# Performance work log

Hardware: AMD Instinct MI355X
Metric: run time of the kernel (lower is better)

## Reference

```python
import jax, jax.numpy as jnp
import numpy as np

B, TQ, TV, D = 8, 256, 512, 128
LN_EPS = 1e-3  # Keras LayerNormalization default epsilon


def setup_inputs() -> dict:
    key = jax.random.key(0)
    k1, k2, k3 = jax.random.split(key, 3)
    x = jax.random.normal(k1, (B, TQ, D), dtype=jnp.float32)
    context = jax.random.normal(k2, (B, TV, D), dtype=jnp.float32)
    scale = jax.random.normal(k3, (D,), dtype=jnp.float32)  # AdditiveAttention use_scale vector
    gamma = jnp.ones((D,), dtype=jnp.float32)
    beta = jnp.zeros((D,), dtype=jnp.float32)
    return {"x": x, "context": context, "scale": scale, "gamma": gamma, "beta": beta}


def reference(x, context, scale, gamma, beta):
    # Bahdanau additive attention: scores[b,i,j] = sum_d scale[d]*tanh(x[b,i,d] + context[b,j,d])
    # [B,TQ,TV,D] broadcasted intermediate, contracted over d with the learned scale vector.
    scores = jnp.einsum("bijd,d->bij", jnp.tanh(x[:, :, None, :] + context[:, None, :, :]), scale)
    weights = jax.nn.softmax(scores, axis=-1)          # [B,TQ,TV]
    attn_out = jnp.einsum("bij,bjd->bid", weights, context)  # weighted sum of values (=context)
    # residual add + LayerNorm over last axis
    y = x + attn_out
    mu = jnp.mean(y, axis=-1, keepdims=True)
    var = jnp.mean(jnp.square(y - mu), axis=-1, keepdims=True)
    out = gamma * (y - mu) * jax.lax.rsqrt(var + LN_EPS) + beta
    return out
```

## Files before the change

### kernel.cpp

```cpp
#include <hip/hip_runtime.h>
#include <math.h>

#define BB 8
#define TQ 256
#define TV 512
#define DD 128
#define TI 4
#define NT 1024
#define LN_EPS 1e-3f

typedef float f4 __attribute__((ext_vector_type(4)));

__global__ __launch_bounds__(256) void prep_kernel(const float* __restrict__ ctx,
                                                   float* __restrict__ F) {
    int idx = blockIdx.x * 256 + threadIdx.x;
    f4 c = ((const f4*)ctx)[idx];
    f4 r;
#pragma unroll
    for (int k = 0; k < 4; ++k) r[k] = __expf(2.0f * c[k]);
    ((f4*)F)[idx] = r;
}

__global__ __launch_bounds__(NT, 8) void attn_kernel(const float* __restrict__ x,
                                                     const float* __restrict__ ctx,
                                                     const float* __restrict__ scale,
                                                     const float* __restrict__ gamma,
                                                     const float* __restrict__ beta,
                                                     const float* __restrict__ F,
                                                     float* __restrict__ out) {
    __shared__ float xs[TI * DD];
    __shared__ f4    txE[DD];
    __shared__ float s2n[DD];
    __shared__ f4    pacc[TV];
    __shared__ f4    wT[TV];
    __shared__ float red[8][TI][DD];
    __shared__ f4    mred[8];
    __shared__ f4    sred[8];
    __shared__ float lnred[8][2];

    const int t  = threadIdx.x;
    const int bg = blockIdx.x;
    const int wg   = (bg & 7) * 64 + (bg >> 3);
    const int b    = wg >> 6;
    const int i0   = (wg & 63) * TI;
    const int wv   = t >> 6;
    const int lane = t & 63;

    if (t < TI * DD) {
        int r = t >> 7, d = t & 127;
        float v = x[(size_t)(b * TQ + i0 + r) * DD + d];
        xs[t] = v;
        txE[d][r] = __expf(2.0f * v);
    }
    if (t >= 512 && t < 512 + DD) s2n[t - 512] = -2.0f * scale[t - 512];
    __syncthreads();

    const int j = t & 511;
    const int h = t >> 9;
    f4 acc = {0.f, 0.f, 0.f, 0.f};
    {
        const f4* Fp = (const f4*)(F + (size_t)(b * TV + j) * DD + h * 64);
#pragma unroll 2
        for (int d4 = 0; d4 < 16; ++d4) {
            f4 Fv = Fp[d4];
#pragma unroll
            for (int k = 0; k < 4; ++k) {
                const int d = h * 64 + d4 * 4 + k;
                f4 E = txE[d];
                float sn = s2n[d];
                f4 den, u;
#pragma unroll
                for (int r = 0; r < TI; ++r) den[r] = fmaf(E[r], Fv[k], 1.0f);
#pragma unroll
                for (int r = 0; r < TI; ++r) u[r] = __builtin_amdgcn_rcpf(den[r]);
#pragma unroll
                for (int r = 0; r < TI; ++r) acc[r] = fmaf(sn, u[r], acc[r]);
            }
        }
    }
    if (h == 1) pacc[j] = acc;
    __syncthreads();
    if (h == 0) {
        f4 o = pacc[j];
#pragma unroll
        for (int r = 0; r < TI; ++r) acc[r] += o[r];
    }

    f4 m = acc;
#pragma unroll
    for (int off = 32; off > 0; off >>= 1) {
#pragma unroll
        for (int r = 0; r < TI; ++r) m[r] = fmaxf(m[r], __shfl_xor(m[r], off));
    }
    if (lane == 0 && wv < 8) mred[wv] = m;
    __syncthreads();
    f4 M = mred[0];
#pragma unroll
    for (int w = 1; w < 8; ++w) {
        f4 o = mred[w];
#pragma unroll
        for (int r = 0; r < TI; ++r) M[r] = fmaxf(M[r], o[r]);
    }
    f4 e;
#pragma unroll
    for (int r = 0; r < TI; ++r) e[r] = __expf(acc[r] - M[r]);
    f4 s = e;
#pragma unroll
    for (int off = 32; off > 0; off >>= 1) {
#pragma unroll
        for (int r = 0; r < TI; ++r) s[r] += __shfl_xor(s[r], off);
    }
    if (lane == 0 && wv < 8) sred[wv] = s;
    __syncthreads();
    f4 S = sred[0];
#pragma unroll
    for (int w = 1; w < 8; ++w) {
        f4 o = sred[w];
#pragma unroll
        for (int r = 0; r < TI; ++r) S[r] += o[r];
    }
    if (h == 0) {
        f4 w4;
#pragma unroll
        for (int r = 0; r < TI; ++r) w4[r] = e[r] * __builtin_amdgcn_rcpf(S[r]);
        wT[j] = w4;
    }
    __syncthreads();

    {
        const int g = t >> 7;
        const int d = t & 127;
        const float* cp = ctx + (size_t)(b * TV + g * 64) * DD + d;
        f4 p = {0.f, 0.f, 0.f, 0.f};
#pragma unroll 4
        for (int jj = 0; jj < 64; ++jj) {
            f4 wj = wT[g * 64 + jj];
            float cv = cp[(size_t)jj * DD];
#pragma unroll
            for (int r = 0; r < TI; ++r) p[r] = fmaf(wj[r], cv, p[r]);
        }
#pragma unroll
        for (int r = 0; r < TI; ++r) red[g][r][d] = p[r];
    }
    __syncthreads();

    {
        const int r = t >> 7;
        const int d = t & 127;
        float y = 0.f;
        if (t < 512) {
            float attn = 0.f;
#pragma unroll
            for (int g = 0; g < 8; ++g) attn += red[g][r][d];
            y = xs[r * DD + d] + attn;
        }
        float s1 = y, s2 = y * y;
#pragma unroll
        for (int off = 32; off > 0; off >>= 1) {
            s1 += __shfl_xor(s1, off);
            s2 += __shfl_xor(s2, off);
        }
        if (lane == 0 && wv < 8) { lnred[wv][0] = s1; lnred[wv][1] = s2; }
        __syncthreads();
        if (t < 512) {
            float S1 = lnred[2 * r][0] + lnred[2 * r + 1][0];
            float S2 = lnred[2 * r][1] + lnred[2 * r + 1][1];
            float mu  = S1 * (1.0f / 128.0f);
            float var = S2 * (1.0f / 128.0f) - mu * mu;
            float inv = rsqrtf(var + LN_EPS);
            out[(size_t)(b * TQ + i0 + r) * DD + d] = gamma[d] * (y - mu) * inv + beta[d];
        }
    }
}

extern "C" void kernel_launch(void* const* d_in, const int* in_sizes, int n_in,
                              void* d_out, int out_size, void* d_ws, size_t ws_size,
                              hipStream_t stream) {
    const float* x     = (const float*)d_in[0];
    const float* ctx   = (const float*)d_in[1];
    const float* scale = (const float*)d_in[2];
    const float* gamma = (const float*)d_in[3];
    const float* beta  = (const float*)d_in[4];
    float* out = (float*)d_out;

    float* F = (float*)d_ws;

    prep_kernel<<<(BB * TV * DD / 4) / 256, 256, 0, stream>>>(ctx, F);
    attn_kernel<<<(BB * TQ) / TI, NT, 0, stream>>>(x, ctx, scale, gamma, beta, F, out);
}
```

Before: 90.91 us.

## Combine four reciprocals into one via common denominator and restructure score split

Groups four d-terms per step and sums their reciprocal contributions over a shared denominator, so one rcp replaces four at the cost of extra multiplies and FMAs. The score work is also re-split: each thread handles two j positions over a quarter of D instead of one j over half of D, with a four-way partial reduction through shared memory. Softmax is reduced only in the first four waves using an online max/sum rescale, which removes one block barrier. The product of four denominators (each 1+e^{2x}e^{2c}) can overflow float range for large inputs, which risks inf/NaN or lost precision.

```diff
diff --git a/kernel.cpp b/kernel.cpp
--- a/kernel.cpp
+++ b/kernel.cpp
@@ -10,6 +10,28 @@
 #define LN_EPS 1e-3f
 
 typedef float f4 __attribute__((ext_vector_type(4)));
+
+static __device__ __forceinline__ f4 vfma_s(f4 a, float s, f4 c) {
+    f4 r;
+    r[0] = fmaf(a[0], s, c[0]); r[1] = fmaf(a[1], s, c[1]);
+    r[2] = fmaf(a[2], s, c[2]); r[3] = fmaf(a[3], s, c[3]);
+    return r;
+}
+static __device__ __forceinline__ f4 vfma_v(f4 a, f4 b, f4 c) {
+    f4 r;
+    r[0] = fmaf(a[0], b[0], c[0]); r[1] = fmaf(a[1], b[1], c[1]);
+    r[2] = fmaf(a[2], b[2], c[2]); r[3] = fmaf(a[3], b[3], c[3]);
+    return r;
+}
+static __device__ __forceinline__ f4 vmul_s(f4 a, float s) {
+    f4 r; r[0] = a[0]*s; r[1] = a[1]*s; r[2] = a[2]*s; r[3] = a[3]*s; return r;
+}
+static __device__ __forceinline__ f4 vrcp(f4 a) {
+    f4 r;
+    r[0] = __builtin_amdgcn_rcpf(a[0]); r[1] = __builtin_amdgcn_rcpf(a[1]);
+    r[2] = __builtin_amdgcn_rcpf(a[2]); r[3] = __builtin_amdgcn_rcpf(a[3]);
+    return r;
+}
 
 __global__ __launch_bounds__(256) void prep_kernel(const float* __restrict__ ctx,
                                                    float* __restrict__ F) {
@@ -30,12 +52,12 @@
                                                      float* __restrict__ out) {
     __shared__ float xs[TI * DD];
     __shared__ f4    txE[DD];
-    __shared__ float s2n[DD];
-    __shared__ f4    pacc[TV];
+    __shared__ f4    s2n4[DD / 4];
+    __shared__ f4    pacc[3][256][2];
     __shared__ f4    wT[TV];
     __shared__ float red[8][TI][DD];
-    __shared__ f4    mred[8];
-    __shared__ f4    sred[8];
+    __shared__ f4    mred[4];
+    __shared__ f4    sred[4];
     __shared__ float lnred[8][2];
 
     const int t  = threadIdx.x;
@@ -52,78 +74,103 @@
         xs[t] = v;
         txE[d][r] = __expf(2.0f * v);
     }
-    if (t >= 512 && t < 512 + DD) s2n[t - 512] = -2.0f * scale[t - 512];
-    __syncthreads();
-
-    const int j = t & 511;
-    const int h = t >> 9;
-    f4 acc = {0.f, 0.f, 0.f, 0.f};
-    {
-        const f4* Fp = (const f4*)(F + (size_t)(b * TV + j) * DD + h * 64);
-#pragma unroll 2
-        for (int d4 = 0; d4 < 16; ++d4) {
-            f4 Fv = Fp[d4];
-#pragma unroll
-            for (int k = 0; k < 4; ++k) {
-                const int d = h * 64 + d4 * 4 + k;
-                f4 E = txE[d];
-                float sn = s2n[d];
-                f4 den, u;
-#pragma unroll
-                for (int r = 0; r < TI; ++r) den[r] = fmaf(E[r], Fv[k], 1.0f);
-#pragma unroll
-                for (int r = 0; r < TI; ++r) u[r] = __builtin_amdgcn_rcpf(den[r]);
-#pragma unroll
-                for (int r = 0; r < TI; ++r) acc[r] = fmaf(sn, u[r], acc[r]);
-            }
-        }
-    }
-    if (h == 1) pacc[j] = acc;
-    __syncthreads();
-    if (h == 0) {
-        f4 o = pacc[j];
-#pragma unroll
-        for (int r = 0; r < TI; ++r) acc[r] += o[r];
-    }
-
-    f4 m = acc;
-#pragma unroll
-    for (int off = 32; off > 0; off >>= 1) {
-#pragma unroll
-        for (int r = 0; r < TI; ++r) m[r] = fmaxf(m[r], __shfl_xor(m[r], off));
-    }
-    if (lane == 0 && wv < 8) mred[wv] = m;
-    __syncthreads();
-    f4 M = mred[0];
-#pragma unroll
-    for (int w = 1; w < 8; ++w) {
-        f4 o = mred[w];
-#pragma unroll
-        for (int r = 0; r < TI; ++r) M[r] = fmaxf(M[r], o[r]);
-    }
-    f4 e;
-#pragma unroll
-    for (int r = 0; r < TI; ++r) e[r] = __expf(acc[r] - M[r]);
-    f4 s = e;
-#pragma unroll
-    for (int off = 32; off > 0; off >>= 1) {
-#pragma unroll
-        for (int r = 0; r < TI; ++r) s[r] += __shfl_xor(s[r], off);
-    }
-    if (lane == 0 && wv < 8) sred[wv] = s;
-    __syncthreads();
-    f4 S = sred[0];
-#pragma unroll
-    for (int w = 1; w < 8; ++w) {
-        f4 o = sred[w];
-#pragma unroll
-        for (int r = 0; r < TI; ++r) S[r] += o[r];
-    }
-    if (h == 0) {
-        f4 w4;
-#pragma unroll
-        for (int r = 0; r < TI; ++r) w4[r] = e[r] * __builtin_amdgcn_rcpf(S[r]);
-        wT[j] = w4;
+    if (t >= 512 && t < 512 + DD / 4) {
+        f4 sv = ((const f4*)scale)[t - 512];
+        s2n4[t - 512] = vmul_s(sv, -2.0f);
+    }
+    __syncthreads();
+
+    const int jj = t & 255;
+    const int q  = t >> 8;
+    const int d0 = q * 32;
+    const f4 one = {1.f, 1.f, 1.f, 1.f};
+
+    auto do_j = [&](int j, f4& a) {
+        const f4* Fp = (const f4*)(F + (size_t)(b * TV + j) * DD + d0);
+#pragma unroll
+        for (int dq = 0; dq < 8; ++dq) {
+            f4 Fv = Fp[dq];
+            const int dbase = d0 + dq * 4;
+            f4 E0 = txE[dbase + 0], E1 = txE[dbase + 1];
+            f4 E2 = txE[dbase + 2], E3 = txE[dbase + 3];
+            f4 sn = s2n4[dbase >> 2];
+            f4 da = vfma_s(E0, Fv[0], one);
+            f4 db = vfma_s(E1, Fv[1], one);
+            f4 ab = da * db;
+            f4 u0 = vmul_s(db, sn[0]);
+            u0 = vfma_s(da, sn[1], u0);
+            f4 dc = vfma_s(E2, Fv[2], one);
+            f4 de = vfma_s(E3, Fv[3], one);
+            f4 ce = dc * de;
+            f4 u1 = vmul_s(de, sn[2]);
+            u1 = vfma_s(dc, sn[3], u1);
+            f4 abce = ab * ce;
+            f4 num = u0 * ce;
+            num = vfma_v(u1, ab, num);
+            f4 rv = vrcp(abce);
+            a = vfma_v(num, rv, a);
+        }
+    };
+    f4 acc0 = {0.f, 0.f, 0.f, 0.f}, acc1 = {0.f, 0.f, 0.f, 0.f};
+    do_j(jj, acc0);
+    do_j(jj + 256, acc1);
+
+    if (q > 0) { pacc[q - 1][jj][0] = acc0; pacc[q - 1][jj][1] = acc1; }
+    __syncthreads();
+
+    f4 m, e0, e1;
+    if (q == 0) {
+#pragma unroll
+        for (int p = 0; p < 3; ++p) {
+            f4 o0 = pacc[p][jj][0], o1 = pacc[p][jj][1];
+#pragma unroll
+            for (int r = 0; r < TI; ++r) { acc0[r] += o0[r]; acc1[r] += o1[r]; }
+        }
+#pragma unroll
+        for (int r = 0; r < TI; ++r) m[r] = fmaxf(acc0[r], acc1[r]);
+#pragma unroll
+        for (int off = 32; off > 0; off >>= 1) {
+#pragma unroll
+            for (int r = 0; r < TI; ++r) m[r] = fmaxf(m[r], __shfl_xor(m[r], off));
+        }
+#pragma unroll
+        for (int r = 0; r < TI; ++r) {
+            e0[r] = __expf(acc0[r] - m[r]);
+            e1[r] = __expf(acc1[r] - m[r]);
+        }
+        f4 s = e0 + e1;
+#pragma unroll
+        for (int off = 32; off > 0; off >>= 1) {
+#pragma unroll
+            for (int r = 0; r < TI; ++r) s[r] += __shfl_xor(s[r], off);
+        }
+        if (lane == 0) { mred[wv] = m; sred[wv] = s; }
+    }
+    __syncthreads();
+    if (q == 0) {
+        f4 M = mred[0];
+#pragma unroll
+        for (int w = 1; w < 4; ++w) {
+            f4 o = mred[w];
+#pragma unroll
+            for (int r = 0; r < TI; ++r) M[r] = fmaxf(M[r], o[r]);
+        }
+        f4 S = {0.f, 0.f, 0.f, 0.f};
+#pragma unroll
+        for (int w = 0; w < 4; ++w) {
+            f4 mw = mred[w], sw = sred[w];
+#pragma unroll
+            for (int r = 0; r < TI; ++r) S[r] += sw[r] * __expf(mw[r] - M[r]);
+        }
+        f4 w0, w1;
+#pragma unroll
+        for (int r = 0; r < TI; ++r) {
+            float inv = __expf(m[r] - M[r]) * __builtin_amdgcn_rcpf(S[r]);
+            w0[r] = e0[r] * inv;
+            w1[r] = e1[r] * inv;
+        }
+        wT[jj] = w0;
+        wT[jj + 256] = w1;
     }
     __syncthreads();
 
@@ -133,11 +180,10 @@
         const float* cp = ctx + (size_t)(b * TV + g * 64) * DD + d;
         f4 p = {0.f, 0.f, 0.f, 0.f};
 #pragma unroll 4
-        for (int jj = 0; jj < 64; ++jj) {
-            f4 wj = wT[g * 64 + jj];
-            float cv = cp[(size_t)jj * DD];
-#pragma unroll
-            for (int r = 0; r < TI; ++r) p[r] = fmaf(wj[r], cv, p[r]);
+        for (int js = 0; js < 64; ++js) {
+            f4 wj = wT[g * 64 + js];
+            float cv = cp[(size_t)js * DD];
+            p = vfma_s(wj, cv, p);
         }
 #pragma unroll
         for (int r = 0; r < TI; ++r) red[g][r][d] = p[r];
```

Result: slower. 322.0 us (+254.2%).

## Pair reciprocals algebraically and precompute transposed exp tables in prep kernel

Applied to the files above, without the earlier changes.

The inner score loop now merges two tanh terms by combining 1/(1+a) and 1/(1+b) into one reciprocal of the product with a weighted numerator, halving the rcp count per dimension. The prep kernel now writes exp(2*context) transposed to [B,D,TV] so per-thread loads are coalesced across j, and it also precomputes exp(2*x) packs and -2*scale, so the attention kernel no longer needs its shared-memory setup or its first barrier. In exchange the E values are read from global or cache instead of LDS, and the product of denominators could overflow float for large inputs.

```diff
diff --git a/kernel.cpp b/kernel.cpp
--- a/kernel.cpp
+++ b/kernel.cpp
@@ -11,72 +11,129 @@
 
 typedef float f4 __attribute__((ext_vector_type(4)));
 
+#define FT_OFF   0
+#define EPK_OFF  (BB * DD * TV)
+#define SN_OFF   (EPK_OFF + BB * TQ * DD)
+
+static __device__ __forceinline__ f4 vfma_s(f4 a, float s, f4 c) {
+    f4 r;
+    r[0] = fmaf(a[0], s, c[0]); r[1] = fmaf(a[1], s, c[1]);
+    r[2] = fmaf(a[2], s, c[2]); r[3] = fmaf(a[3], s, c[3]);
+    return r;
+}
+static __device__ __forceinline__ f4 vfma_v(f4 a, f4 b, f4 c) {
+    f4 r;
+    r[0] = fmaf(a[0], b[0], c[0]); r[1] = fmaf(a[1], b[1], c[1]);
+    r[2] = fmaf(a[2], b[2], c[2]); r[3] = fmaf(a[3], b[3], c[3]);
+    return r;
+}
+static __device__ __forceinline__ f4 vmul_s(f4 a, float s) {
+    f4 r; r[0] = a[0]*s; r[1] = a[1]*s; r[2] = a[2]*s; r[3] = a[3]*s; return r;
+}
+static __device__ __forceinline__ f4 vrcp(f4 a) {
+    f4 r;
+    r[0] = __builtin_amdgcn_rcpf(a[0]); r[1] = __builtin_amdgcn_rcpf(a[1]);
+    r[2] = __builtin_amdgcn_rcpf(a[2]); r[3] = __builtin_amdgcn_rcpf(a[3]);
+    return r;
+}
+
 __global__ __launch_bounds__(256) void prep_kernel(const float* __restrict__ ctx,
-                                                   float* __restrict__ F) {
-    int idx = blockIdx.x * 256 + threadIdx.x;
-    f4 c = ((const f4*)ctx)[idx];
-    f4 r;
-#pragma unroll
-    for (int k = 0; k < 4; ++k) r[k] = __expf(2.0f * c[k]);
-    ((f4*)F)[idx] = r;
+                                                   const float* __restrict__ x,
+                                                   const float* __restrict__ scale,
+                                                   float* __restrict__ ws) {
+    float* FT  = ws + FT_OFF;
+    f4*    Epk = (f4*)(ws + EPK_OFF);
+    f4*    sn4 = (f4*)(ws + SN_OFF);
+    const int t = threadIdx.x;
+    const int blk = blockIdx.x;
+    if (blk < 64) {
+        __shared__ float tile[64][DD + 1];
+        const int b = blk >> 3, j0 = (blk & 7) * 64;
+        const f4* c4 = (const f4*)ctx;
+#pragma unroll
+        for (int k = 0; k < 8; ++k) {
+            int idx = k * 256 + t;
+            int jr = idx >> 5, d4 = idx & 31;
+            f4 c = c4[(size_t)(b * TV + j0 + jr) * (DD / 4) + d4];
+#pragma unroll
+            for (int i = 0; i < 4; ++i) tile[jr][d4 * 4 + i] = __expf(2.0f * c[i]);
+        }
+        __syncthreads();
+        const int jl = t & 63, dh = t >> 6;
+#pragma unroll
+        for (int dd = 0; dd < 32; ++dd) {
+            int d = dh * 32 + dd;
+            FT[(size_t)(b * DD + d) * TV + j0 + jl] = tile[jl][d];
+        }
+    } else {
+        int idx = (blk - 64) * 256 + t;
+        int d = idx & 127, ig = idx >> 7;
+        f4 e;
+#pragma unroll
+        for (int r = 0; r < 4; ++r)
+            e[r] = __expf(2.0f * x[(size_t)(ig * 4 + r) * DD + d]);
+        Epk[idx] = e;
+        if (blk == 64 && t < DD / 4) {
+            f4 s = ((const f4*)scale)[t];
+            f4 o; o[0] = -2.f*s[0]; o[1] = -2.f*s[1]; o[2] = -2.f*s[2]; o[3] = -2.f*s[3];
+            sn4[t] = o;
+        }
+    }
 }
 
 __global__ __launch_bounds__(NT, 8) void attn_kernel(const float* __restrict__ x,
                                                      const float* __restrict__ ctx,
-                                                     const float* __restrict__ scale,
                                                      const float* __restrict__ gamma,
                                                      const float* __restrict__ beta,
-                                                     const float* __restrict__ F,
+                                                     const float* __restrict__ ws,
                                                      float* __restrict__ out) {
-    __shared__ float xs[TI * DD];
-    __shared__ f4    txE[DD];
-    __shared__ float s2n[DD];
     __shared__ f4    pacc[TV];
     __shared__ f4    wT[TV];
     __shared__ float red[8][TI][DD];
-    __shared__ f4    mred[8];
-    __shared__ f4    sred[8];
+    __shared__ f4    mred[8], sred[8];
     __shared__ float lnred[8][2];
+
+    const float* FT  = ws + FT_OFF;
+    const f4*    Epk = (const f4*)(ws + EPK_OFF);
+    const f4*    sn4 = (const f4*)(ws + SN_OFF);
 
     const int t  = threadIdx.x;
     const int bg = blockIdx.x;
     const int wg   = (bg & 7) * 64 + (bg >> 3);
     const int b    = wg >> 6;
-    const int i0   = (wg & 63) * TI;
+    const int ig   = wg & 63;
+    const int i0   = ig * TI;
     const int wv   = t >> 6;
     const int lane = t & 63;
 
-    if (t < TI * DD) {
-        int r = t >> 7, d = t & 127;
-        float v = x[(size_t)(b * TQ + i0 + r) * DD + d];
-        xs[t] = v;
-        txE[d][r] = __expf(2.0f * v);
-    }
-    if (t >= 512 && t < 512 + DD) s2n[t - 512] = -2.0f * scale[t - 512];
-    __syncthreads();
-
     const int j = t & 511;
     const int h = t >> 9;
+
+    const float* Fp = FT + (size_t)(b * DD + h * 64) * TV + j;
+    const f4*    Ep = Epk + (size_t)(b * 64 + ig) * DD + h * 64;
+    const f4 one = {1.f, 1.f, 1.f, 1.f};
     f4 acc = {0.f, 0.f, 0.f, 0.f};
-    {
-        const f4* Fp = (const f4*)(F + (size_t)(b * TV + j) * DD + h * 64);
-#pragma unroll 2
-        for (int d4 = 0; d4 < 16; ++d4) {
-            f4 Fv = Fp[d4];
-#pragma unroll
-            for (int k = 0; k < 4; ++k) {
-                const int d = h * 64 + d4 * 4 + k;
-                f4 E = txE[d];
-                float sn = s2n[d];
-                f4 den, u;
-#pragma unroll
-                for (int r = 0; r < TI; ++r) den[r] = fmaf(E[r], Fv[k], 1.0f);
-#pragma unroll
-                for (int r = 0; r < TI; ++r) u[r] = __builtin_amdgcn_rcpf(den[r]);
-#pragma unroll
-                for (int r = 0; r < TI; ++r) acc[r] = fmaf(sn, u[r], acc[r]);
-            }
-        }
+#pragma unroll 4
+    for (int dq = 0; dq < 16; ++dq) {
+        f4 sq = sn4[h * 16 + dq];
+        f4 e0 = Ep[dq * 4 + 0], e1 = Ep[dq * 4 + 1];
+        f4 e2 = Ep[dq * 4 + 2], e3 = Ep[dq * 4 + 3];
+        float f0 = Fp[(size_t)(dq * 4 + 0) * TV];
+        float f1 = Fp[(size_t)(dq * 4 + 1) * TV];
+        float f2 = Fp[(size_t)(dq * 4 + 2) * TV];
+        float f3 = Fp[(size_t)(dq * 4 + 3) * TV];
+        f4 da = vfma_s(e0, f0, one);
+        f4 db = vfma_s(e1, f1, one);
+        f4 pr = da * db;
+        f4 nu = vmul_s(db, sq[0]);
+        nu = vfma_s(da, sq[1], nu);
+        acc = vfma_v(nu, vrcp(pr), acc);
+        f4 dc = vfma_s(e2, f2, one);
+        f4 de = vfma_s(e3, f3, one);
+        f4 p2 = dc * de;
+        f4 n2 = vmul_s(de, sq[2]);
+        n2 = vfma_s(dc, sq[3], n2);
+        acc = vfma_v(n2, vrcp(p2), acc);
     }
     if (h == 1) pacc[j] = acc;
     __syncthreads();
@@ -92,7 +149,7 @@
 #pragma unroll
         for (int r = 0; r < TI; ++r) m[r] = fmaxf(m[r], __shfl_xor(m[r], off));
     }
-    if (lane == 0 && wv < 8) mred[wv] = m;
+    if (h == 0 && lane == 0) mred[wv] = m;
     __syncthreads();
     f4 M = mred[0];
 #pragma unroll
@@ -110,7 +167,7 @@
 #pragma unroll
         for (int r = 0; r < TI; ++r) s[r] += __shfl_xor(s[r], off);
     }
-    if (lane == 0 && wv < 8) sred[wv] = s;
+    if (h == 0 && lane == 0) sred[wv] = s;
     __syncthreads();
     f4 S = sred[0];
 #pragma unroll
@@ -133,11 +190,10 @@
         const float* cp = ctx + (size_t)(b * TV + g * 64) * DD + d;
         f4 p = {0.f, 0.f, 0.f, 0.f};
 #pragma unroll 4
-        for (int jj = 0; jj < 64; ++jj) {
-            f4 wj = wT[g * 64 + jj];
-            float cv = cp[(size_t)jj * DD];
-#pragma unroll
-            for (int r = 0; r < TI; ++r) p[r] = fmaf(wj[r], cv, p[r]);
+        for (int js = 0; js < 64; ++js) {
+            f4 wj = wT[g * 64 + js];
+            float cv = cp[(size_t)js * DD];
+            p = vfma_s(wj, cv, p);
         }
 #pragma unroll
         for (int r = 0; r < TI; ++r) red[g][r][d] = p[r];
@@ -145,14 +201,14 @@
     __syncthreads();
 
     {
-        const int r = t >> 7;
-        const int d = t & 127;
+        const int r  = t >> 7;
+        const int dd = t & 127;
         float y = 0.f;
         if (t < 512) {
             float attn = 0.f;
 #pragma unroll
-            for (int g = 0; g < 8; ++g) attn += red[g][r][d];
-            y = xs[r * DD + d] + attn;
+            for (int g2 = 0; g2 < 8; ++g2) attn += red[g2][r][dd];
+            y = x[(size_t)(b * TQ + i0 + r) * DD + dd] + attn;
         }
         float s1 = y, s2 = y * y;
 #pragma unroll
@@ -168,7 +224,7 @@
             float mu  = S1 * (1.0f / 128.0f);
             float var = S2 * (1.0f / 128.0f) - mu * mu;
             float inv = rsqrtf(var + LN_EPS);
-            out[(size_t)(b * TQ + i0 + r) * DD + d] = gamma[d] * (y - mu) * inv + beta[d];
+            out[(size_t)(b * TQ + i0 + r) * DD + dd] = gamma[dd] * (y - mu) * inv + beta[dd];
         }
     }
 }
@@ -182,9 +238,8 @@
     const float* gamma = (const float*)d_in[3];
     const float* beta  = (const float*)d_in[4];
     float* out = (float*)d_out;
-
-    float* F = (float*)d_ws;
-
-    prep_kernel<<<(BB * TV * DD / 4) / 256, 256, 0, stream>>>(ctx, F);
-    attn_kernel<<<(BB * TQ) / TI, NT, 0, stream>>>(x, ctx, scale, gamma, beta, F, out);
-}
+    float* ws  = (float*)d_ws;
+
+    prep_kernel<<<320, 256, 0, stream>>>(ctx, x, scale, ws);
+    attn_kernel<<<(BB * TQ) / TI, NT, 0, stream>>>(x, ctx, gamma, beta, ws, out);
+}
```

Measured after the change: 96.25 us. 1.06x slower.

## Pair reciprocals, process two query rows per block with transposed F layout

Applied to the files above, without the earlier changes.

Restructures the additive-attention kernel so each block handles 2 query rows with 512 threads, one per context position, covering the full D range per thread. It removes the two-half partial-sum exchange. Adjacent tanh terms are combined algebraically (sa/da + sb/db = (sa·db + sb·da)/(da·db)), which halves the reciprocal count. The prep kernel writes exp(2·ctx) in a d-group-major layout so that per-thread loads of F are coalesced across j. The softmax uses an online-style combine of per-wave max/sum, which saves one barrier. Risks: twice as many blocks, each with less reuse of F across rows, and possible overflow in the product of denominators.

```diff
diff --git a/kernel.cpp b/kernel.cpp
--- a/kernel.cpp
+++ b/kernel.cpp
@@ -5,171 +5,178 @@
 #define TQ 256
 #define TV 512
 #define DD 128
-#define TI 4
-#define NT 1024
 #define LN_EPS 1e-3f
 
+typedef float f2 __attribute__((ext_vector_type(2)));
 typedef float f4 __attribute__((ext_vector_type(4)));
 
-__global__ __launch_bounds__(256) void prep_kernel(const float* __restrict__ ctx,
-                                                   float* __restrict__ F) {
-    int idx = blockIdx.x * 256 + threadIdx.x;
-    f4 c = ((const f4*)ctx)[idx];
-    f4 r;
-#pragma unroll
-    for (int k = 0; k < 4; ++k) r[k] = __expf(2.0f * c[k]);
-    ((f4*)F)[idx] = r;
+static __device__ __forceinline__ f2 fma2s(f2 a, float s, f2 c) {
+    f2 r; r[0] = fmaf(a[0], s, c[0]); r[1] = fmaf(a[1], s, c[1]); return r;
+}
+static __device__ __forceinline__ f2 fma2v(f2 a, f2 b, f2 c) {
+    f2 r; r[0] = fmaf(a[0], b[0], c[0]); r[1] = fmaf(a[1], b[1], c[1]); return r;
+}
+static __device__ __forceinline__ f2 rcp2(f2 a) {
+    f2 r; r[0] = __builtin_amdgcn_rcpf(a[0]); r[1] = __builtin_amdgcn_rcpf(a[1]); return r;
 }
 
-__global__ __launch_bounds__(NT, 8) void attn_kernel(const float* __restrict__ x,
-                                                     const float* __restrict__ ctx,
-                                                     const float* __restrict__ scale,
-                                                     const float* __restrict__ gamma,
-                                                     const float* __restrict__ beta,
-                                                     const float* __restrict__ F,
-                                                     float* __restrict__ out) {
-    __shared__ float xs[TI * DD];
-    __shared__ f4    txE[DD];
-    __shared__ float s2n[DD];
-    __shared__ f4    pacc[TV];
-    __shared__ f4    wT[TV];
-    __shared__ float red[8][TI][DD];
-    __shared__ f4    mred[8];
-    __shared__ f4    sred[8];
-    __shared__ float lnred[8][2];
+__global__ __launch_bounds__(256) void prep_kernel(const float* __restrict__ ctx,
+                                                   float* __restrict__ ws) {
+    int idx = blockIdx.x * 256 + threadIdx.x;
+    int d4 = idx & 31, j = (idx >> 5) & 511, b = idx >> 14;
+    f4 c = ((const f4*)ctx)[idx];
+    f4 e;
+#pragma unroll
+    for (int i = 0; i < 4; ++i) e[i] = __expf(2.0f * c[i]);
+    int g = d4 >> 2, q = d4 & 3;
+    ((f4*)ws)[(((b * 8 + g) * 512) + j) * 4 + q] = e;
+}
+
+__global__ __launch_bounds__(512, 8) void attn_kernel(const float* __restrict__ x,
+                                                      const float* __restrict__ ctx,
+                                                      const float* __restrict__ scale,
+                                                      const float* __restrict__ gamma,
+                                                      const float* __restrict__ beta,
+                                                      const float* __restrict__ ws,
+                                                      float* __restrict__ out) {
+    __shared__ f2    E2[DD];
+    __shared__ f4    sn4[DD / 4];
+    __shared__ f2    wT[TV];
+    __shared__ float red[8][2][DD];
+    __shared__ f2    mred[8], sred[8];
+    __shared__ float lnred[4][2];
 
     const int t  = threadIdx.x;
     const int bg = blockIdx.x;
-    const int wg   = (bg & 7) * 64 + (bg >> 3);
-    const int b    = wg >> 6;
-    const int i0   = (wg & 63) * TI;
+    const int wg   = (bg & 7) * 128 + (bg >> 3);
+    const int b    = wg >> 7;
+    const int i0   = (wg & 127) * 2;
     const int wv   = t >> 6;
     const int lane = t & 63;
 
-    if (t < TI * DD) {
-        int r = t >> 7, d = t & 127;
-        float v = x[(size_t)(b * TQ + i0 + r) * DD + d];
-        xs[t] = v;
-        txE[d][r] = __expf(2.0f * v);
+    if (t < DD) {
+        float v0 = x[(size_t)(b * TQ + i0) * DD + t];
+        float v1 = x[(size_t)(b * TQ + i0 + 1) * DD + t];
+        f2 e; e[0] = __expf(2.0f * v0); e[1] = __expf(2.0f * v1);
+        E2[t] = e;
+    } else if (t < DD + DD / 4) {
+        f4 s = ((const f4*)scale)[t - DD];
+        f4 o; o[0] = -2.f * s[0]; o[1] = -2.f * s[1]; o[2] = -2.f * s[2]; o[3] = -2.f * s[3];
+        sn4[t - DD] = o;
     }
-    if (t >= 512 && t < 512 + DD) s2n[t - 512] = -2.0f * scale[t - 512];
     __syncthreads();
 
-    const int j = t & 511;
-    const int h = t >> 9;
-    f4 acc = {0.f, 0.f, 0.f, 0.f};
-    {
-        const f4* Fp = (const f4*)(F + (size_t)(b * TV + j) * DD + h * 64);
+    const int j = t;
+    const f4* F4 = (const f4*)ws;
+    const int fbase = b * 16384 + j * 4;
+    const f2 one2 = {1.f, 1.f};
+    f2 acc = {0.f, 0.f};
 #pragma unroll 2
-        for (int d4 = 0; d4 < 16; ++d4) {
-            f4 Fv = Fp[d4];
+    for (int g = 0; g < 8; ++g) {
+        f4 F0 = F4[fbase + g * 2048 + 0];
+        f4 F1 = F4[fbase + g * 2048 + 1];
+        f4 F2 = F4[fbase + g * 2048 + 2];
+        f4 F3 = F4[fbase + g * 2048 + 3];
+        const f4 Fv[4] = {F0, F1, F2, F3};
 #pragma unroll
-            for (int k = 0; k < 4; ++k) {
-                const int d = h * 64 + d4 * 4 + k;
-                f4 E = txE[d];
-                float sn = s2n[d];
-                f4 den, u;
-#pragma unroll
-                for (int r = 0; r < TI; ++r) den[r] = fmaf(E[r], Fv[k], 1.0f);
-#pragma unroll
-                for (int r = 0; r < TI; ++r) u[r] = __builtin_amdgcn_rcpf(den[r]);
-#pragma unroll
-                for (int r = 0; r < TI; ++r) acc[r] = fmaf(sn, u[r], acc[r]);
-            }
+        for (int q = 0; q < 4; ++q) {
+            f4 sn = sn4[g * 4 + q];
+            const int db0 = g * 16 + q * 4;
+            f2 Ea = E2[db0 + 0], Eb = E2[db0 + 1], Ec = E2[db0 + 2], Ed = E2[db0 + 3];
+            f4 Fq = Fv[q];
+            f2 da = fma2s(Ea, Fq[0], one2);
+            f2 db = fma2s(Eb, Fq[1], one2);
+            f2 nu = db * sn[0];
+            nu = fma2s(da, sn[1], nu);
+            acc = fma2v(nu, rcp2(da * db), acc);
+            f2 dc = fma2s(Ec, Fq[2], one2);
+            f2 de = fma2s(Ed, Fq[3], one2);
+            f2 n2 = de * sn[2];
+            n2 = fma2s(dc, sn[3], n2);
+            acc = fma2v(n2, rcp2(dc * de), acc);
         }
     }
-    if (h == 1) pacc[j] = acc;
-    __syncthreads();
-    if (h == 0) {
-        f4 o = pacc[j];
-#pragma unroll
-        for (int r = 0; r < TI; ++r) acc[r] += o[r];
-    }
 
-    f4 m = acc;
+    f2 m = acc;
 #pragma unroll
     for (int off = 32; off > 0; off >>= 1) {
-#pragma unroll
-        for (int r = 0; r < TI; ++r) m[r] = fmaxf(m[r], __shfl_xor(m[r], off));
+        m[0] = fmaxf(m[0], __shfl_xor(m[0], off));
+        m[1] = fmaxf(m[1], __shfl_xor(m[1], off));
     }
-    if (lane == 0 && wv < 8) mred[wv] = m;
-    __syncthreads();
-    f4 M = mred[0];
-#pragma unroll
-    for (int w = 1; w < 8; ++w) {
-        f4 o = mred[w];
-#pragma unroll
-        for (int r = 0; r < TI; ++r) M[r] = fmaxf(M[r], o[r]);
-    }
-    f4 e;
-#pragma unroll
-    for (int r = 0; r < TI; ++r) e[r] = __expf(acc[r] - M[r]);
-    f4 s = e;
+    f2 e;
+    e[0] = __expf(acc[0] - m[0]);
+    e[1] = __expf(acc[1] - m[1]);
+    f2 s = e;
 #pragma unroll
     for (int off = 32; off > 0; off >>= 1) {
+        s[0] += __shfl_xor(s[0], off);
+        s[1] += __shfl_xor(s[1], off);
+    }
+    if (lane == 0) { mred[wv] = m; sred[wv] = s; }
+    __syncthreads();
+    {
+        f2 M = mred[0];
 #pragma unroll
-        for (int r = 0; r < TI; ++r) s[r] += __shfl_xor(s[r], off);
-    }
-    if (lane == 0 && wv < 8) sred[wv] = s;
-    __syncthreads();
-    f4 S = sred[0];
+        for (int w = 1; w < 8; ++w) {
+            f2 o = mred[w];
+            M[0] = fmaxf(M[0], o[0]); M[1] = fmaxf(M[1], o[1]);
+        }
+        f2 S = {0.f, 0.f};
 #pragma unroll
-    for (int w = 1; w < 8; ++w) {
-        f4 o = sred[w];
-#pragma unroll
-        for (int r = 0; r < TI; ++r) S[r] += o[r];
-    }
-    if (h == 0) {
-        f4 w4;
-#pragma unroll
-        for (int r = 0; r < TI; ++r) w4[r] = e[r] * __builtin_amdgcn_rcpf(S[r]);
-        wT[j] = w4;
+        for (int w = 0; w < 8; ++w) {
+            f2 mw = mred[w], sw = sred[w];
+            S[0] += sw[0] * __expf(mw[0] - M[0]);
+            S[1] += sw[1] * __expf(mw[1] - M[1]);
+        }
+        f2 w2;
+        w2[0] = __expf(acc[0] - M[0]) * __builtin_amdgcn_rcpf(S[0]);
+        w2[1] = __expf(acc[1] - M[1]) * __builtin_amdgcn_rcpf(S[1]);
+        wT[j] = w2;
     }
     __syncthreads();
 
     {
-        const int g = t >> 7;
-        const int d = t & 127;
-        const float* cp = ctx + (size_t)(b * TV + g * 64) * DD + d;
+        const int g  = t >> 6;
+        const int d2 = t & 63;
+        const f2* cp = (const f2*)ctx + (size_t)(b * TV + g * 64) * 64 + d2;
         f4 p = {0.f, 0.f, 0.f, 0.f};
 #pragma unroll 4
-        for (int jj = 0; jj < 64; ++jj) {
-            f4 wj = wT[g * 64 + jj];
-            float cv = cp[(size_t)jj * DD];
-#pragma unroll
-            for (int r = 0; r < TI; ++r) p[r] = fmaf(wj[r], cv, p[r]);
+        for (int js = 0; js < 64; ++js) {
+            f2 wj = wT[g * 64 + js];
+            f2 cv = cp[(size_t)js * 64];
+            p[0] = fmaf(wj[0], cv[0], p[0]);
+            p[1] = fmaf(wj[0], cv[1], p[1]);
+            p[2] = fmaf(wj[1], cv[0], p[2]);
+            p[3] = fmaf(wj[1], cv[1], p[3]);
         }
-#pragma unroll
-        for (int r = 0; r < TI; ++r) red[g][r][d] = p[r];
+        *(f2*)&red[g][0][2 * d2] = f2{p[0], p[1]};
+        *(f2*)&red[g][1][2 * d2] = f2{p[2], p[3]};
     }
     __syncthreads();
 
-    {
-        const int r = t >> 7;
-        const int d = t & 127;
-        float y = 0.f;
-        if (t < 512) {
-            float attn = 0.f;
+    float y = 0.f;
+    const int r = t >> 7, dd = t & 127;
+    if (t < 256) {
+        float attn = 0.f;
 #pragma unroll
-            for (int g = 0; g < 8; ++g) attn += red[g][r][d];
-            y = xs[r * DD + d] + attn;
-        }
-        float s1 = y, s2 = y * y;
+        for (int g2 = 0; g2 < 8; ++g2) attn += red[g2][r][dd];
+        y = x[(size_t)(b * TQ + i0 + r) * DD + dd] + attn;
+    }
+    float s1 = y, s2 = y * y;
 #pragma unroll
-        for (int off = 32; off > 0; off >>= 1) {
-            s1 += __shfl_xor(s1, off);
-            s2 += __shfl_xor(s2, off);
-        }
-        if (lane == 0 && wv < 8) { lnred[wv][0] = s1; lnred[wv][1] = s2; }
-        __syncthreads();
-        if (t < 512) {
-            float S1 = lnred[2 * r][0] + lnred[2 * r + 1][0];
-            float S2 = lnred[2 * r][1] + lnred[2 * r + 1][1];
-            float mu  = S1 * (1.0f / 128.0f);
-            float var = S2 * (1.0f / 128.0f) - mu * mu;
-            float inv = rsqrtf(var + LN_EPS);
-            out[(size_t)(b * TQ + i0 + r) * DD + d] = gamma[d] * (y - mu) * inv + beta[d];
-        }
+    for (int off = 32; off > 0; off >>= 1) {
+        s1 += __shfl_xor(s1, off);
+        s2 += __shfl_xor(s2, off);
+    }
+    if (t < 256 && lane == 0) { lnred[wv][0] = s1; lnred[wv][1] = s2; }
+    __syncthreads();
+    if (t < 256) {
+        float S1 = lnred[2 * r][0] + lnred[2 * r + 1][0];
+        float S2 = lnred[2 * r][1] + lnred[2 * r + 1][1];
+        float mu  = S1 * (1.0f / 128.0f);
+        float var = S2 * (1.0f / 128.0f) - mu * mu;
+        float inv = rsqrtf(var + LN_EPS);
+        out[(size_t)(b * TQ + i0 + r) * DD + dd] = gamma[dd] * (y - mu) * inv + beta[dd];
     }
 }
 
@@ -182,9 +189,8 @@
     const float* gamma = (const float*)d_in[3];
     const float* beta  = (const float*)d_in[4];
     float* out = (float*)d_out;
+    float* ws  = (float*)d_ws;
 
-    float* F = (float*)d_ws;
-
-    prep_kernel<<<(BB * TV * DD / 4) / 256, 256, 0, stream>>>(ctx, F);
-    attn_kernel<<<(BB * TQ) / TI, NT, 0, stream>>>(x, ctx, scale, gamma, beta, F, out);
+    prep_kernel<<<512, 256, 0, stream>>>(ctx, ws);
+    attn_kernel<<<1024, 512, 0, stream>>>(x, ctx, scale, gamma, beta, ws, out);
 }
```

After: 132.3 us. 1.46x slower.
